# Kernel tuning notes

Hardware: AMD Instinct MI355X
Metric: run time of the kernel (lower is better)

Reference implementation:

```python
import jax, jax.numpy as jnp
import numpy as np

B, T, D, H = 8, 1024, 768, 12
HD = D // H          # 64 head dim
WINDOW = 768         # sliding-window width hardcoded in the block
EPS = 1e-5

def _layer_norm(x, w, b):
    mu = jnp.mean(x, axis=-1, keepdims=True)
    var = jnp.mean(jnp.square(x - mu), axis=-1, keepdims=True)
    return (x - mu) * jax.lax.rsqrt(var + EPS) * w + b

def setup_inputs() -> dict:
    key = jax.random.key(0)
    ks = jax.random.split(key, 16)
    s = 0.02
    return {
        "x": jax.random.normal(ks[0], (B, T, D), jnp.float32),
        "attn_mask": jnp.ones((B, T), jnp.int32),
        "ln1_w": jnp.ones((D,), jnp.float32),
        "ln1_b": jnp.zeros((D,), jnp.float32),
        "w_attn": jax.random.normal(ks[1], (D, 3 * D), jnp.float32) * s,
        "b_attn": jnp.zeros((3 * D,), jnp.float32),
        "w_proj": jax.random.normal(ks[2], (D, D), jnp.float32) * s,
        "b_proj": jnp.zeros((D,), jnp.float32),
        "ln2_w": jnp.ones((D,), jnp.float32),
        "ln2_b": jnp.zeros((D,), jnp.float32),
        "w_fc": jax.random.normal(ks[3], (D, 4 * D), jnp.float32) * s,
        "b_fc": jnp.zeros((4 * D,), jnp.float32),
        "w_fc_proj": jax.random.normal(ks[4], (4 * D, D), jnp.float32) * s,
        "b_fc_proj": jnp.zeros((D,), jnp.float32),
    }

def reference(x, attn_mask, ln1_w, ln1_b, w_attn, b_attn, w_proj, b_proj,
              ln2_w, ln2_b, w_fc, b_fc, w_fc_proj, b_fc_proj):
    dtype = x.dtype
    # --- attention sub-block ---
    x1 = _layer_norm(x, ln1_w, ln1_b)
    qkv = x1 @ w_attn + b_attn                       # [B,T,3D]
    q, k, v = jnp.split(qkv, 3, axis=-1)
    q = q.reshape(B, T, H, HD).transpose(0, 2, 1, 3)  # [B,H,T,HD]
    k = k.reshape(B, T, H, HD).transpose(0, 2, 1, 3)
    v = v.reshape(B, T, H, HD).transpose(0, 2, 1, 3)
    # causal + sliding-window + padding mask (additive bias, as in source)
    i = jnp.arange(T)[:, None]
    j = jnp.arange(T)[None, :]
    keep = (j <= i) & (j >= i - WINDOW + 1)           # [T,T]
    keep = keep[None, None] & (attn_mask.astype(bool))[:, None, None, :]  # [B,1,T,T]
    mask_bias = jnp.where(keep, jnp.zeros((), dtype), jnp.full((), jnp.finfo(dtype).min, dtype))
    scale = 1.0 / np.sqrt(HD)
    scores = jnp.einsum('bhqd,bhkd->bhqk', q, k) * scale + mask_bias
    probs = jax.nn.softmax(scores, axis=-1)
    attn = jnp.einsum('bhqk,bhkd->bhqd', probs, v)    # [B,H,T,HD]
    attn = attn.transpose(0, 2, 1, 3).reshape(B, T, D)
    a = attn @ w_proj + b_proj
    x = x + a
    # --- MLP sub-block ---
    x3 = _layer_norm(x, ln2_w, ln2_b)
    h = jax.nn.gelu(x3 @ w_fc + b_fc, approximate=False)
    m = h @ w_fc_proj + b_fc_proj
    return x + m
```

## Files before the change

### kernel.cpp

```cpp
#include <hip/hip_runtime.h>
#include <hip/hip_bf16.h>
#include <math.h>

#define NB 8
#define NT 1024
#define ND 768
#define NH 12
#define HD 64
#define WINDOW 768
#define LN_EPS 1e-5f
#define NEGF -3.4028234663852886e38f
#define SCL2 0.18033688011112042f

static const int BT = NB * NT;

typedef __bf16 bf16x8 __attribute__((ext_vector_type(8)));
typedef float  f32x4  __attribute__((ext_vector_type(4)));
typedef unsigned short ushort_t;

__device__ __forceinline__ unsigned short f2bf(float f) {
    __hip_bfloat16 h = __float2bfloat16(f);
    return __builtin_bit_cast(unsigned short, h);
}

__device__ __forceinline__ void load_lds16(const void* g, void* l) {
    __builtin_amdgcn_global_load_lds((const __attribute__((address_space(1))) unsigned int*)g,
                                     (__attribute__((address_space(3))) unsigned int*)l,
                                     16, 0, 0);
}

__global__ __launch_bounds__(256) void transpose_all(const float* __restrict__ w0, ushort_t* __restrict__ t0v,
                                                     const float* __restrict__ w1, ushort_t* __restrict__ t1v,
                                                     const float* __restrict__ w2, ushort_t* __restrict__ t2v,
                                                     const float* __restrict__ w3, ushort_t* __restrict__ t3v) {
    int bid = blockIdx.x;
    const float* w; ushort_t* wt; int K, N;
    if (bid < 1728)                    { w = w0; wt = t0v; K = 768;  N = 2304; }
    else if ((bid -= 1728) < 576)      { w = w1; wt = t1v; K = 768;  N = 768;  }
    else if ((bid -= 576) < 2304)      { w = w2; wt = t2v; K = 768;  N = 3072; }
    else       { bid -= 2304;            w = w3; wt = t3v; K = 3072; N = 768;  }
    const int nxt = N / 32;
    const int n0 = (bid % nxt) * 32, k0 = (bid / nxt) * 32;
    __shared__ float t[32][33];
    const int tx = threadIdx.x & 31, ty = threadIdx.x >> 5;
    for (int r = ty; r < 32; r += 8)
        t[r][tx] = w[(size_t)(k0 + r) * N + n0 + tx];
    __syncthreads();
    for (int r = ty; r < 32; r += 8)
        wt[(size_t)(n0 + r) * K + k0 + tx] = f2bf(t[tx][r]);
}

__global__ __launch_bounds__(256) void transpose_v(const ushort_t* __restrict__ qkvb,
                                                   ushort_t* __restrict__ vT) {
    const int t0 = blockIdx.x * 64;
    const int h = blockIdx.y, b = blockIdx.z;
    __shared__ ushort_t sm[64 * 72];
    const int tid = threadIdx.x;
    #pragma unroll
    for (int p = 0; p < 2; p++) {
        int idx = p * 256 + tid;
        int r = idx >> 3, c = idx & 7;
        *(bf16x8*)&sm[r * 72 + c * 8] =
            *(const bf16x8*)(qkvb + (size_t)(b * NT + t0 + r) * (3 * ND) + 2 * ND + h * HD + c * 8);
    }
    __syncthreads();
    #pragma unroll
    for (int p = 0; p < 2; p++) {
        int idx = p * 256 + tid;
        int d = idx >> 3, c2 = idx & 7;
        ushort_t tmp[8];
        #pragma unroll
        for (int j = 0; j < 8; j++) {
            int kp = c2 * 8 + j;
            int key = ((kp & 1) << 4) | ((kp >> 1) & 15) | (kp & 32);
            tmp[j] = sm[key * 72 + d];
        }
        *(bf16x8*)(vT + ((size_t)((b * NH + h) * HD + d)) * NT + t0 + c2 * 8) = *(bf16x8*)tmp;
    }
}

__global__ __launch_bounds__(256) void ln_kernel(const float* __restrict__ x,
                                                 const float* __restrict__ w,
                                                 const float* __restrict__ b,
                                                 ushort_t* __restrict__ out) {
    const int row  = blockIdx.x * 4 + (threadIdx.x >> 6);
    const int lane = threadIdx.x & 63;
    const float* xr = x + (size_t)row * ND;

    float4 v[3];
    #pragma unroll
    for (int s = 0; s < 3; s++) v[s] = *(const float4*)(xr + s * 256 + lane * 4);

    float sum = 0.f;
    #pragma unroll
    for (int s = 0; s < 3; s++) sum += v[s].x + v[s].y + v[s].z + v[s].w;
    #pragma unroll
    for (int off = 1; off < 64; off <<= 1) sum += __shfl_xor(sum, off, 64);
    const float mu = sum * (1.0f / ND);

    float var = 0.f;
    #pragma unroll
    for (int s = 0; s < 3; s++) {
        float a0 = v[s].x - mu, a1 = v[s].y - mu, a2 = v[s].z - mu, a3 = v[s].w - mu;
        var += a0 * a0 + a1 * a1 + a2 * a2 + a3 * a3;
    }
    #pragma unroll
    for (int off = 1; off < 64; off <<= 1) var += __shfl_xor(var, off, 64);
    const float rstd = rsqrtf(var * (1.0f / ND) + LN_EPS);

    #pragma unroll
    for (int s = 0; s < 3; s++) {
        const int col = s * 256 + lane * 4;
        float4 w4 = *(const float4*)(w + col);
        float4 b4 = *(const float4*)(b + col);
        ushort4 r;
        r.x = f2bf((v[s].x - mu) * rstd * w4.x + b4.x);
        r.y = f2bf((v[s].y - mu) * rstd * w4.y + b4.y);
        r.z = f2bf((v[s].z - mu) * rstd * w4.z + b4.z);
        r.w = f2bf((v[s].w - mu) * rstd * w4.w + b4.w);
        *(ushort4*)(out + (size_t)row * ND + col) = r;
    }
}

template <int EPI>
__global__ __launch_bounds__(256) void gemm_bt(const ushort_t* __restrict__ A,
                                               const ushort_t* __restrict__ Bt,
                                               const float* __restrict__ bias,
                                               const float* __restrict__ resid,
                                               void* __restrict__ Cout,
                                               int M, int N, int K) {
    __shared__ __align__(16) ushort_t smem[2][2][128 * 32];

    const int tid  = threadIdx.x;
    const int bm   = blockIdx.y * 128;
    const int bn   = blockIdx.x * 128;
    const int lane = tid & 63;
    const int wave = tid >> 6;
    const int wm   = (wave & 1) * 64;
    const int wn   = (wave >> 1) * 64;
    const int fcol = lane & 15;
    const int quad = lane >> 4;

    f32x4 acc[4][4] = {};

    const int srow = tid >> 2, scg = (tid & 3) * 8;

    auto issue = [&](int k0, int buf) {
        #pragma unroll
        for (int p = 0; p < 2; p++) {
            const int row = srow + p * 64;
            const int flat = (p * 256 + tid) * 8;
            load_lds16(A  + (size_t)(bm + row) * K + k0 + scg, &smem[buf][0][flat]);
            load_lds16(Bt + (size_t)(bn + row) * K + k0 + scg, &smem[buf][1][flat]);
        }
    };

    issue(0, 0);
    const int KT = K >> 5;
    for (int kt = 0; kt < KT; kt++) {
        const int cur = kt & 1;
        __syncthreads();
        if (kt + 1 < KT) issue((kt + 1) << 5, cur ^ 1);

        bf16x8 a[4], b[4];
        #pragma unroll
        for (int i = 0; i < 4; i++)
            a[i] = *(const bf16x8*)&smem[cur][0][(wm + i * 16 + fcol) * 32 + quad * 8];
        #pragma unroll
        for (int j = 0; j < 4; j++)
            b[j] = *(const bf16x8*)&smem[cur][1][(wn + j * 16 + fcol) * 32 + quad * 8];
        #pragma unroll
        for (int i = 0; i < 4; i++)
            #pragma unroll
            for (int j = 0; j < 4; j++)
                acc[i][j] = __builtin_amdgcn_mfma_f32_16x16x32_bf16(a[i], b[j], acc[i][j], 0, 0, 0);
    }

    if (EPI == 1) {
        #pragma unroll
        for (int j = 0; j < 4; j++) {
            const int gcol = bn + wn + j * 16 + fcol;
            const float bs = bias[gcol];
            #pragma unroll
            for (int i = 0; i < 4; i++) {
                #pragma unroll
                for (int r = 0; r < 4; r++) {
                    const int grow = bm + wm + i * 16 + quad * 4 + r;
                    float val = acc[i][j][r] + bs + resid[(size_t)grow * N + gcol];
                    ((float*)Cout)[(size_t)grow * N + gcol] = val;
                }
            }
        }
    } else {
        __syncthreads();
        ushort_t* Cs = &smem[0][0][0] + wave * (64 * 40);
        #pragma unroll
        for (int hh = 0; hh < 2; hh++) {
            #pragma unroll
            for (int jj = 0; jj < 2; jj++) {
                const int j = hh * 2 + jj;
                const float bs = bias[bn + wn + j * 16 + fcol];
                #pragma unroll
                for (int i = 0; i < 4; i++) {
                    #pragma unroll
                    for (int r = 0; r < 4; r++) {
                        float val = acc[i][j][r] + bs;
                        if (EPI == 2) {
                            float y = 0.7978845608028654f * (val + 0.044715f * val * val * val);
                            float t = 1.0f - 2.0f / (1.0f + __expf(2.0f * y));
                            val = 0.5f * val * (1.0f + t);
                        }
                        const int lr = i * 16 + quad * 4 + r;
                        Cs[lr * 40 + jj * 16 + fcol] = f2bf(val);
                    }
                }
            }
            #pragma unroll
            for (int p = 0; p < 4; p++) {
                const int cid = p * 64 + lane;
                const int lr = cid >> 2, ck = cid & 3;
                bf16x8 vv = *(const bf16x8*)&Cs[lr * 40 + ck * 8];
                *(bf16x8*)((ushort_t*)Cout + (size_t)(bm + wm + lr) * N + bn + wn + hh * 32 + ck * 8) = vv;
            }
        }
    }
}

template <int EPI>
__global__ __launch_bounds__(512, 2) void gemm256(const ushort_t* __restrict__ A,
                                                  const ushort_t* __restrict__ Bt,
                                                  const float* __restrict__ bias,
                                                  ushort_t* __restrict__ Cout,
                                                  int N, int K) {
    extern __shared__ __align__(16) ushort_t lds[];

    const int tid  = threadIdx.x;
    const int lane = tid & 63;
    const int wave = tid >> 6;
    const int wr   = wave >> 2;
    const int wn   = wave & 3;
    const int fcol = lane & 15;
    const int quad = lane >> 4;
    const int bm   = blockIdx.y * 256;
    const int bn   = blockIdx.x * 256;
    const int KT   = K >> 6;
    const int NIT  = KT >> 1;

    f32x4 acc[8][4] = {};
    bf16x8 ra[4][2];
    bf16x8 rb0[2][2], rb1[2][2];

    ushort_t* const Ab = lds;
    ushort_t* const Bb = lds + 32768;

    auto stA = [&](int kt, int h) {
        ushort_t* dst = Ab + ((((kt & 1) << 1) | h) << 13);
        const int kk = (kt < KT ? kt : 0) << 6;
        #pragma unroll
        for (int p = 0; p < 2; p++) {
            const int f = (p << 9) + tid;
            const int r = f >> 3, c = (f & 7) ^ (r & 7);
            const int gr = bm + ((r >> 6) << 7) + (h << 6) + (r & 63);
            load_lds16(A + (size_t)gr * K + kk + c * 8, dst + f * 8);
        }
    };
    auto stB = [&](int kt, int h) {
        ushort_t* dst = Bb + ((((kt & 1) << 1) | h) << 13);
        const int kk = (kt < KT ? kt : 0) << 6;
        #pragma unroll
        for (int p = 0; p < 2; p++) {
            const int f = (p << 9) + tid;
            const int r = f >> 3, c = (f & 7) ^ (r & 7);
            const int gr = bn + ((r >> 5) << 6) + (h << 5) + (r & 31);
            load_lds16(Bt + (size_t)gr * K + kk + c * 8, dst + f * 8);
        }
    };

#define SOFF(r, c) ((((r) << 3) + (((c) ^ ((r) & 7)))) << 3)
#define LOAD_A(PAR, MH) { ushort_t* s_ = Ab + ((((PAR) << 1) | (MH)) << 13);        \
    _Pragma("unroll") for (int i2 = 0; i2 < 4; i2++)                                 \
    _Pragma("unroll") for (int ks = 0; ks < 2; ks++)                                 \
        ra[i2][ks] = *(const bf16x8*)&s_[SOFF(wr * 64 + i2 * 16 + fcol, ks * 4 + quad)]; }
#define LOAD_B(PAR, NH, RB) { ushort_t* s_ = Bb + ((((PAR) << 1) | (NH)) << 13);     \
    _Pragma("unroll") for (int j2 = 0; j2 < 2; j2++)                                 \
    _Pragma("unroll") for (int ks = 0; ks < 2; ks++)                                 \
        RB[j2][ks] = *(const bf16x8*)&s_[SOFF(wn * 32 + j2 * 16 + fcol, ks * 4 + quad)]; }
#define MMA(MH, NH, RB) { __builtin_amdgcn_s_setprio(1);                             \
    _Pragma("unroll") for (int i2 = 0; i2 < 4; i2++)                                 \
    _Pragma("unroll") for (int j2 = 0; j2 < 2; j2++)                                 \
    _Pragma("unroll") for (int ks = 0; ks < 2; ks++)                                 \
        acc[(MH) * 4 + i2][(NH) * 2 + j2] = __builtin_amdgcn_mfma_f32_16x16x32_bf16( \
            ra[i2][ks], RB[j2][ks], acc[(MH) * 4 + i2][(NH) * 2 + j2], 0, 0, 0);     \
    __builtin_amdgcn_s_setprio(0); }
#define BAR() __builtin_amdgcn_s_barrier()

    stA(0, 0); stB(0, 0); stB(0, 1); stA(0, 1);
    stA(1, 0); stB(1, 0); stB(1, 1);
    asm volatile("s_waitcnt vmcnt(6)" ::: "memory");
    BAR();

    for (int it = 0; it < NIT; ++it) {
        const int E = it << 1, O = E + 1;
        LOAD_A(0, 0); LOAD_B(0, 0, rb0);
        stA(O, 1);
        BAR(); MMA(0, 0, rb0); BAR();

        LOAD_B(0, 1, rb1);
        stA(E + 2, 0);
        BAR(); MMA(0, 1, rb1); BAR();

        LOAD_A(0, 1);
        stB(E + 2, 0);
        BAR(); MMA(1, 1, rb1); BAR();

        stB(E + 2, 1);
        asm volatile("s_waitcnt vmcnt(6)" ::: "memory");
        BAR(); MMA(1, 0, rb0); BAR();

        LOAD_A(1, 0); LOAD_B(1, 0, rb0);
        stA(E + 2, 1);
        BAR(); MMA(0, 0, rb0); BAR();

        LOAD_B(1, 1, rb1);
        stA(O + 2, 0);
        BAR(); MMA(0, 1, rb1); BAR();

        LOAD_A(1, 1);
        stB(O + 2, 0);
        BAR(); MMA(1, 1, rb1); BAR();

        stB(O + 2, 1);
        asm volatile("s_waitcnt vmcnt(6)" ::: "memory");
        BAR(); MMA(1, 0, rb0); BAR();
    }

    asm volatile("s_waitcnt vmcnt(0)" ::: "memory");
    BAR();

    ushort_t* Cs = lds + wave * (64 * 72);
    #pragma unroll
    for (int h = 0; h < 2; h++) {
        #pragma unroll
        for (int j = 0; j < 4; j++) {
            const float bs = bias[bn + wn * 64 + j * 16 + fcol];
            #pragma unroll
            for (int i2 = 0; i2 < 4; i2++) {
                #pragma unroll
                for (int r = 0; r < 4; r++) {
                    float val = acc[h * 4 + i2][j][r] + bs;
                    if (EPI == 2) {
                        float y = 0.7978845608028654f * (val + 0.044715f * val * val * val);
                        float t = 1.0f - 2.0f / (1.0f + __expf(2.0f * y));
                        val = 0.5f * val * (1.0f + t);
                    }
                    Cs[(i2 * 16 + quad * 4 + r) * 72 + j * 16 + fcol] = f2bf(val);
                }
            }
        }
        #pragma unroll
        for (int p = 0; p < 8; p++) {
            const int cid = (p << 6) + lane;
            const int lr = cid >> 3, ck = cid & 7;
            bf16x8 vv = *(const bf16x8*)&Cs[lr * 72 + ck * 8];
            *(bf16x8*)(Cout + (size_t)(bm + wr * 128 + h * 64 + lr) * N + bn + wn * 64 + ck * 8) = vv;
        }
    }
#undef SOFF
#undef LOAD_A
#undef LOAD_B
#undef MMA
#undef BAR
}

__global__ __launch_bounds__(256) void flash_attn_mfma(const ushort_t* __restrict__ qkvb,
                                                       const ushort_t* __restrict__ vT,
                                                       const int* __restrict__ amask,
                                                       ushort_t* __restrict__ out) {
    const int qt = 15 - blockIdx.x;
    const int h  = blockIdx.y;
    const int b  = blockIdx.z;
    const int q0 = qt * 64;

    __shared__ __align__(16) ushort_t QPs[64 * 64];
    __shared__ __align__(16) ushort_t Ks[2][64 * 64];
    __shared__ __align__(16) ushort_t Vts[2][64 * 64];

    const int tid  = threadIdx.x;
    const int lane = tid & 63;
    const int wave = tid >> 6;
    const int fcol = lane & 15;
    const int quad = lane >> 4;
    const int wq0  = wave * 16;

    #pragma unroll
    for (int p = 0; p < 2; p++) {
        int flat = p * 256 + tid;
        int r = flat >> 3, c = (flat & 7) ^ (r & 7);
        load_lds16(qkvb + (size_t)(b * NT + q0 + r) * (3 * ND) + h * HD + c * 8, &QPs[flat * 8]);
    }
    __syncthreads();

    bf16x8 aQ[2];
    {
        const int qr = wq0 + fcol;
        #pragma unroll
        for (int ks = 0; ks < 2; ks++) {
            int c = ks * 4 + quad;
            aQ[ks] = *(const bf16x8*)&QPs[qr * 64 + ((c ^ (qr & 7)) * 8)];
        }
    }

    bf16x8 bones;
    #pragma unroll
    for (int i = 0; i < 8; i++) bones[i] = (__bf16)1.0f;

    auto issueKV = [&](int cch, int buf) {
        const int kbase = cch * 64;
        #pragma unroll
        for (int p = 0; p < 2; p++) {
            int flat = p * 256 + tid;
            int r = flat >> 3, c = (flat & 7) ^ (r & 7);
            load_lds16(qkvb + (size_t)(b * NT + kbase + r) * (3 * ND) + ND + h * HD + c * 8,
                       &Ks[buf][flat * 8]);
            load_lds16(vT + ((size_t)((b * NH + h) * HD + r)) * NT + kbase + c * 8,
                       &Vts[buf][flat * 8]);
        }
    };

    f32x4 oacc[4] = {};
    f32x4 lacc = {};

    const int c_lo = (qt > 12) ? (qt - 12) : 0;
    issueKV(c_lo, 0);
    for (int cch = c_lo; cch <= qt; cch++) {
        const int cur = (cch - c_lo) & 1;
        const int kbase = cch * 64;
        __syncthreads();
        if (cch + 1 <= qt) issueKV(cch + 1, cur ^ 1);

        int am[4];
        #pragma unroll
        for (int jn = 0; jn < 4; jn++) am[jn] = amask[b * NT + kbase + jn * 16 + fcol];
        const int amok_lane = (am[0] != 0) & (am[1] != 0) & (am[2] != 0) & (am[3] != 0);
        const bool fast = (cch < qt) && (cch >= qt - 11) && __all(amok_lane);

        f32x4 sc[4] = {};
        #pragma unroll
        for (int ks = 0; ks < 2; ks++) {
            #pragma unroll
            for (int jn = 0; jn < 4; jn++) {
                const int kr = jn * 16 + fcol;
                bf16x8 bk = *(const bf16x8*)&Ks[cur][kr * 64 + (((ks * 4 + quad) ^ (kr & 7)) * 8)];
                sc[jn] = __builtin_amdgcn_mfma_f32_16x16x32_bf16(aQ[ks], bk, sc[jn], 0, 0, 0);
            }
        }

        float pvv[4][4];
        if (fast) {
            #pragma unroll
            for (int jn = 0; jn < 4; jn++)
                #pragma unroll
                for (int r = 0; r < 4; r++)
                    pvv[jn][r] = __builtin_amdgcn_exp2f(sc[jn][r] * SCL2);
        } else {
            #pragma unroll
            for (int jn = 0; jn < 4; jn++) {
                const int jg = kbase + jn * 16 + fcol;
                const bool amok = (am[jn] != 0);
                #pragma unroll
                for (int r = 0; r < 4; r++) {
                    const int ig = q0 + wq0 + quad * 4 + r;
                    bool keep = (jg <= ig) && (jg >= ig - (WINDOW - 1)) && amok;
                    float s = keep ? sc[jn][r] * SCL2 : -1e38f;
                    pvv[jn][r] = __builtin_amdgcn_exp2f(s);
                }
            }
        }

        #pragma unroll
        for (int half = 0; half < 2; half++) {
            const int cbase = half * 4 + (fcol >> 2);
            const int off = (fcol & 3) * 2;
            #pragma unroll
            for (int r = 0; r < 4; r++) {
                const int row = wq0 + quad * 4 + r;
                unsigned int pk = (unsigned int)f2bf(pvv[half * 2][r]) |
                                  ((unsigned int)f2bf(pvv[half * 2 + 1][r]) << 16);
                *(unsigned int*)&QPs[row * 64 + ((cbase ^ (row & 7)) * 8) + off] = pk;
            }
        }

        #pragma unroll
        for (int ks = 0; ks < 2; ks++) {
            const int pr = wq0 + fcol;
            bf16x8 ap = *(const bf16x8*)&QPs[pr * 64 + (((ks * 4 + quad) ^ (pr & 7)) * 8)];
            lacc = __builtin_amdgcn_mfma_f32_16x16x32_bf16(ap, bones, lacc, 0, 0, 0);
            #pragma unroll
            for (int jd = 0; jd < 4; jd++) {
                const int vr = jd * 16 + fcol;
                bf16x8 bv = *(const bf16x8*)&Vts[cur][vr * 64 + (((ks * 4 + quad) ^ (vr & 7)) * 8)];
                oacc[jd] = __builtin_amdgcn_mfma_f32_16x16x32_bf16(ap, bv, oacc[jd], 0, 0, 0);
            }
        }
    }

    #pragma unroll
    for (int r = 0; r < 4; r++) {
        const float inv = 1.0f / lacc[r];
        const size_t row = (size_t)(b * NT + q0 + wq0 + quad * 4 + r);
        #pragma unroll
        for (int jd = 0; jd < 4; jd++)
            out[row * ND + h * HD + jd * 16 + fcol] = f2bf(oacc[jd][r] * inv);
    }
}

extern "C" void kernel_launch(void* const* d_in, const int* in_sizes, int n_in,
                              void* d_out, int out_size, void* d_ws, size_t ws_size,
                              hipStream_t stream) {
    const float* x        = (const float*)d_in[0];
    const int*   amask    = (const int*)  d_in[1];
    const float* ln1_w    = (const float*)d_in[2];
    const float* ln1_b    = (const float*)d_in[3];
    const float* w_attn   = (const float*)d_in[4];
    const float* b_attn   = (const float*)d_in[5];
    const float* w_proj   = (const float*)d_in[6];
    const float* b_proj   = (const float*)d_in[7];
    const float* ln2_w    = (const float*)d_in[8];
    const float* ln2_b    = (const float*)d_in[9];
    const float* w_fc     = (const float*)d_in[10];
    const float* b_fc     = (const float*)d_in[11];
    const float* w_fcp    = (const float*)d_in[12];
    const float* b_fcp    = (const float*)d_in[13];
    float* out = (float*)d_out;

    ushort_t* ws = (ushort_t*)d_ws;
    ushort_t* qkvb   = ws;
    ushort_t* x1b    = qkvb + (size_t)BT * 3 * ND;
    ushort_t* attn_b = x1b + (size_t)BT * ND;
    ushort_t* hbuf   = attn_b + (size_t)BT * ND;
    ushort_t* vTb    = hbuf + (size_t)BT * 4 * ND;
    ushort_t* wA_T   = vTb + (size_t)BT * ND;
    ushort_t* wP_T   = wA_T + (size_t)2304 * 768;
    ushort_t* wF_T   = wP_T + (size_t)768 * 768;
    ushort_t* wFP_T  = wF_T + (size_t)3072 * 768;

    static bool attr_set = false;
    if (!attr_set) {
        hipFuncSetAttribute((const void*)gemm256<0>, hipFuncAttributeMaxDynamicSharedMemorySize, 131072);
        hipFuncSetAttribute((const void*)gemm256<2>, hipFuncAttributeMaxDynamicSharedMemorySize, 131072);
        attr_set = true;
    }

    transpose_all<<<6912, 256, 0, stream>>>(w_attn, wA_T, w_proj, wP_T, w_fc, wF_T, w_fcp, wFP_T);

    ln_kernel<<<BT / 4, 256, 0, stream>>>(x, ln1_w, ln1_b, x1b);
    gemm256<0><<<dim3(2304 / 256, BT / 256), 512, 131072, stream>>>(x1b, wA_T, b_attn, qkvb, 3 * ND, ND);
    transpose_v<<<dim3(16, NH, NB), 256, 0, stream>>>(qkvb, vTb);
    flash_attn_mfma<<<dim3(16, NH, NB), 256, 0, stream>>>(qkvb, vTb, amask, attn_b);
    gemm_bt<1><<<dim3(768 / 128, BT / 128), 256, 0, stream>>>(attn_b, wP_T, b_proj, x, out, BT, ND, ND);
    ln_kernel<<<BT / 4, 256, 0, stream>>>(out, ln2_w, ln2_b, x1b);
    gemm256<2><<<dim3(3072 / 256, BT / 256), 512, 131072, stream>>>(x1b, wF_T, b_fc, hbuf, 4 * ND, ND);
    gemm_bt<1><<<dim3(768 / 128, BT / 128), 256, 0, stream>>>(hbuf, wFP_T, b_fcp, out, out, BT, ND, 4 * ND);
}
```

Measured before the change: 386.2 us.

## Tune gemm256 scheduling: inline-asm LDS reads, sched barriers, XCD-aware block swizzle, constexpr dims

Makes N and K template constants so loop bounds and strides are known at compile time, and keeps the main loop rolled. LDS fragment reads now go through inline ds_read_b128 asm, with explicit lgkmcnt waits and sched_barrier fences around each MFMA phase so the compiler cannot interleave or reorder them. Workgroup IDs are remapped with an 8-way swizzle, aimed at MI355X's multiple chiplets (XCDs) so neighbouring tiles share cache. These changes target instruction scheduling and cache locality in the two large GEMMs, but forcing lgkmcnt(0) before every MFMA burst may remove some latency overlap.

```diff
diff --git a/kernel.cpp b/kernel.cpp
--- a/kernel.cpp
+++ b/kernel.cpp
@@ -27,6 +27,13 @@
     __builtin_amdgcn_global_load_lds((const __attribute__((address_space(1))) unsigned int*)g,
                                      (__attribute__((address_space(3))) unsigned int*)l,
                                      16, 0, 0);
+}
+
+__device__ __forceinline__ bf16x8 ds_read16(const ushort_t* p) {
+    bf16x8 r;
+    unsigned a = (unsigned)(size_t)(const __attribute__((address_space(3))) ushort_t*)p;
+    asm volatile("ds_read_b128 %0, %1" : "=v"(r) : "v"(a));
+    return r;
 }
 
 __global__ __launch_bounds__(256) void transpose_all(const float* __restrict__ w0, ushort_t* __restrict__ t0v,
@@ -226,12 +233,11 @@
     }
 }
 
-template <int EPI>
+template <int EPI, int NN, int KK>
 __global__ __launch_bounds__(512, 2) void gemm256(const ushort_t* __restrict__ A,
                                                   const ushort_t* __restrict__ Bt,
                                                   const float* __restrict__ bias,
-                                                  ushort_t* __restrict__ Cout,
-                                                  int N, int K) {
+                                                  ushort_t* __restrict__ Cout) {
     extern __shared__ __align__(16) ushort_t lds[];
 
     const int tid  = threadIdx.x;
@@ -241,10 +247,16 @@
     const int wn   = wave & 3;
     const int fcol = lane & 15;
     const int quad = lane >> 4;
-    const int bm   = blockIdx.y * 256;
-    const int bn   = blockIdx.x * 256;
-    const int KT   = K >> 6;
-    const int NIT  = KT >> 1;
+
+    const int nwg  = gridDim.x * gridDim.y;
+    const int flat = blockIdx.y * gridDim.x + blockIdx.x;
+    const int q8   = nwg >> 3;
+    const int swz  = (flat & 7) * q8 + (flat >> 3);
+    const int bm   = (swz / gridDim.x) * 256;
+    const int bn   = (swz % gridDim.x) * 256;
+
+    constexpr int KT  = KK >> 6;
+    constexpr int NIT = KT >> 1;
 
     f32x4 acc[8][4] = {};
     bf16x8 ra[4][2];
@@ -261,7 +273,7 @@
             const int f = (p << 9) + tid;
             const int r = f >> 3, c = (f & 7) ^ (r & 7);
             const int gr = bm + ((r >> 6) << 7) + (h << 6) + (r & 63);
-            load_lds16(A + (size_t)gr * K + kk + c * 8, dst + f * 8);
+            load_lds16(A + (size_t)gr * KK + kk + c * 8, dst + f * 8);
         }
     };
     auto stB = [&](int kt, int h) {
@@ -272,70 +284,77 @@
             const int f = (p << 9) + tid;
             const int r = f >> 3, c = (f & 7) ^ (r & 7);
             const int gr = bn + ((r >> 5) << 6) + (h << 5) + (r & 31);
-            load_lds16(Bt + (size_t)gr * K + kk + c * 8, dst + f * 8);
+            load_lds16(Bt + (size_t)gr * KK + kk + c * 8, dst + f * 8);
         }
     };
 
 #define SOFF(r, c) ((((r) << 3) + (((c) ^ ((r) & 7)))) << 3)
-#define LOAD_A(PAR, MH) { ushort_t* s_ = Ab + ((((PAR) << 1) | (MH)) << 13);        \
+#define LOAD_A(PAR, MH) { const ushort_t* s_ = Ab + ((((PAR) << 1) | (MH)) << 13);   \
     _Pragma("unroll") for (int i2 = 0; i2 < 4; i2++)                                 \
     _Pragma("unroll") for (int ks = 0; ks < 2; ks++)                                 \
-        ra[i2][ks] = *(const bf16x8*)&s_[SOFF(wr * 64 + i2 * 16 + fcol, ks * 4 + quad)]; }
-#define LOAD_B(PAR, NH, RB) { ushort_t* s_ = Bb + ((((PAR) << 1) | (NH)) << 13);     \
+        ra[i2][ks] = ds_read16(&s_[SOFF(wr * 64 + i2 * 16 + fcol, ks * 4 + quad)]); }
+#define LOAD_B(PAR, NH, RB) { const ushort_t* s_ = Bb + ((((PAR) << 1) | (NH)) << 13); \
     _Pragma("unroll") for (int j2 = 0; j2 < 2; j2++)                                 \
     _Pragma("unroll") for (int ks = 0; ks < 2; ks++)                                 \
-        RB[j2][ks] = *(const bf16x8*)&s_[SOFF(wn * 32 + j2 * 16 + fcol, ks * 4 + quad)]; }
-#define MMA(MH, NH, RB) { __builtin_amdgcn_s_setprio(1);                             \
+        RB[j2][ks] = ds_read16(&s_[SOFF(wn * 32 + j2 * 16 + fcol, ks * 4 + quad)]); }
+#define MMA(MH, NH, RB) {                                                            \
+    __builtin_amdgcn_s_barrier();                                                    \
+    asm volatile("s_waitcnt lgkmcnt(0)" ::: "memory");                               \
+    __builtin_amdgcn_sched_barrier(0);                                               \
+    __builtin_amdgcn_s_setprio(1);                                                   \
     _Pragma("unroll") for (int i2 = 0; i2 < 4; i2++)                                 \
     _Pragma("unroll") for (int j2 = 0; j2 < 2; j2++)                                 \
     _Pragma("unroll") for (int ks = 0; ks < 2; ks++)                                 \
         acc[(MH) * 4 + i2][(NH) * 2 + j2] = __builtin_amdgcn_mfma_f32_16x16x32_bf16( \
             ra[i2][ks], RB[j2][ks], acc[(MH) * 4 + i2][(NH) * 2 + j2], 0, 0, 0);     \
-    __builtin_amdgcn_s_setprio(0); }
-#define BAR() __builtin_amdgcn_s_barrier()
+    __builtin_amdgcn_s_setprio(0);                                                   \
+    __builtin_amdgcn_sched_barrier(0);                                               \
+    __builtin_amdgcn_s_barrier(); }
+#define VMW6() asm volatile("s_waitcnt vmcnt(6)" ::: "memory")
 
     stA(0, 0); stB(0, 0); stB(0, 1); stA(0, 1);
     stA(1, 0); stB(1, 0); stB(1, 1);
-    asm volatile("s_waitcnt vmcnt(6)" ::: "memory");
-    BAR();
-
+    VMW6();
+    __builtin_amdgcn_s_barrier();
+
+    #pragma unroll 1
     for (int it = 0; it < NIT; ++it) {
         const int E = it << 1, O = E + 1;
         LOAD_A(0, 0); LOAD_B(0, 0, rb0);
         stA(O, 1);
-        BAR(); MMA(0, 0, rb0); BAR();
+        MMA(0, 0, rb0);
 
         LOAD_B(0, 1, rb1);
         stA(E + 2, 0);
-        BAR(); MMA(0, 1, rb1); BAR();
+        MMA(0, 1, rb1);
 
         LOAD_A(0, 1);
         stB(E + 2, 0);
-        BAR(); MMA(1, 1, rb1); BAR();
+        MMA(1, 1, rb1);
 
         stB(E + 2, 1);
-        asm volatile("s_waitcnt vmcnt(6)" ::: "memory");
-        BAR(); MMA(1, 0, rb0); BAR();
+        VMW6();
+        MMA(1, 0, rb0);
 
         LOAD_A(1, 0); LOAD_B(1, 0, rb0);
         stA(E + 2, 1);
-        BAR(); MMA(0, 0, rb0); BAR();
+        MMA(0, 0, rb0);
 
         LOAD_B(1, 1, rb1);
         stA(O + 2, 0);
-        BAR(); MMA(0, 1, rb1); BAR();
+        MMA(0, 1, rb1);
 
         LOAD_A(1, 1);
         stB(O + 2, 0);
-        BAR(); MMA(1, 1, rb1); BAR();
+        MMA(1, 1, rb1);
 
         stB(O + 2, 1);
-        asm volatile("s_waitcnt vmcnt(6)" ::: "memory");
-        BAR(); MMA(1, 0, rb0); BAR();
+        VMW6();
+        MMA(1, 0, rb0);
     }
 
     asm volatile("s_waitcnt vmcnt(0)" ::: "memory");
-    BAR();
+    __builtin_amdgcn_s_barrier();
 
     ushort_t* Cs = lds + wave * (64 * 72);
     #pragma unroll
@@ -362,14 +381,14 @@
             const int cid = (p << 6) + lane;
             const int lr = cid >> 3, ck = cid & 7;
             bf16x8 vv = *(const bf16x8*)&Cs[lr * 72 + ck * 8];
-            *(bf16x8*)(Cout + (size_t)(bm + wr * 128 + h * 64 + lr) * N + bn + wn * 64 + ck * 8) = vv;
+            *(bf16x8*)(Cout + (size_t)(bm + wr * 128 + h * 64 + lr) * NN + bn + wn * 64 + ck * 8) = vv;
         }
     }
 #undef SOFF
 #undef LOAD_A
 #undef LOAD_B
 #undef MMA
-#undef BAR
+#undef VMW6
 }
 
 __global__ __launch_bounds__(256) void flash_attn_mfma(const ushort_t* __restrict__ qkvb,
@@ -546,19 +565,19 @@
 
     static bool attr_set = false;
     if (!attr_set) {
-        hipFuncSetAttribute((const void*)gemm256<0>, hipFuncAttributeMaxDynamicSharedMemorySize, 131072);
-        hipFuncSetAttribute((const void*)gemm256<2>, hipFuncAttributeMaxDynamicSharedMemorySize, 131072);
+        hipFuncSetAttribute((const void*)gemm256<0, 2304, 768>, hipFuncAttributeMaxDynamicSharedMemorySize, 131072);
+        hipFuncSetAttribute((const void*)gemm256<2, 3072, 768>, hipFuncAttributeMaxDynamicSharedMemorySize, 131072);
         attr_set = true;
     }
 
     transpose_all<<<6912, 256, 0, stream>>>(w_attn, wA_T, w_proj, wP_T, w_fc, wF_T, w_fcp, wFP_T);
 
     ln_kernel<<<BT / 4, 256, 0, stream>>>(x, ln1_w, ln1_b, x1b);
-    gemm256<0><<<dim3(2304 / 256, BT / 256), 512, 131072, stream>>>(x1b, wA_T, b_attn, qkvb, 3 * ND, ND);
+    gemm256<0, 2304, 768><<<dim3(2304 / 256, BT / 256), 512, 131072, stream>>>(x1b, wA_T, b_attn, qkvb);
     transpose_v<<<dim3(16, NH, NB), 256, 0, stream>>>(qkvb, vTb);
     flash_attn_mfma<<<dim3(16, NH, NB), 256, 0, stream>>>(qkvb, vTb, amask, attn_b);
     gemm_bt<1><<<dim3(768 / 128, BT / 128), 256, 0, stream>>>(attn_b, wP_T, b_proj, x, out, BT, ND, ND);
     ln_kernel<<<BT / 4, 256, 0, stream>>>(out, ln2_w, ln2_b, x1b);
-    gemm256<2><<<dim3(3072 / 256, BT / 256), 512, 131072, stream>>>(x1b, wF_T, b_fc, hbuf, 4 * ND, ND);
+    gemm256<2, 3072, 768><<<dim3(3072 / 256, BT / 256), 512, 131072, stream>>>(x1b, wF_T, b_fc, hbuf);
     gemm_bt<1><<<dim3(768 / 128, BT / 128), 256, 0, stream>>>(hbuf, wFP_T, b_fcp, out, out, BT, ND, 4 * ND);
 }
```

Result: no change. 382.3 us (-1.0%).
